# Performance work log

Measured on AMD Instinct MI355X. Metric: run time of the kernel, lower is better.

Reference implementation:

```python
import jax, jax.numpy as jnp
import numpy as np


def setup_inputs() -> dict:
    key = jax.random.key(0)
    k1, k2, k3 = jax.random.split(key, 3)
    N, F, C, E = 100000, 256, 64, 3200000
    x = jax.random.normal(k1, (N, F), dtype=jnp.float32)
    edge_index = jax.random.randint(k2, (2, E), 0, N, dtype=jnp.int64)
    W = jax.random.normal(k3, (F, C), dtype=jnp.float32) * (1.0 / np.sqrt(F))
    b = jnp.zeros((C,), dtype=jnp.float32)
    return {"x": x, "edge_index": edge_index, "W": W, "b": b}


def reference(x, edge_index, W, b):
    N = x.shape[0]
    # Linear transform first (GCNConv: x @ W)
    xw = x @ W  # [N, C]
    # gcn_norm: add self-loops with weight 1
    loops = jnp.arange(N, dtype=edge_index.dtype)
    src = jnp.concatenate([edge_index[0], loops])
    dst = jnp.concatenate([edge_index[1], loops])
    ones = jnp.ones(src.shape[0], dtype=xw.dtype)
    deg = jax.ops.segment_sum(ones, dst, num_segments=N)  # in-degree incl. self-loop
    deg_inv_sqrt = jnp.where(deg > 0, jax.lax.rsqrt(deg), 0.0)
    norm = deg_inv_sqrt[src] * deg_inv_sqrt[dst]  # [E+N]
    # Message: norm * x_j, then MEAN aggregation over destinations (aggr='mean')
    msg = xw[src] * norm[:, None]  # [E+N, C]
    agg = jax.ops.segment_sum(msg, dst, num_segments=N)  # [N, C]
    cnt = jnp.maximum(deg, 1.0)  # number of incoming messages per node
    out = agg / cnt[:, None] + b
    return jax.nn.log_softmax(out, axis=1)
```

## Files before the change

### kernel.cpp

```cpp
#include <hip/hip_runtime.h>


#define C_DIM 64
#define F_DIM 256
#define TILE 128
#define BIN_PT 16
#define BIN_TILE_E 4096
#define SORT_CAP 6144

typedef __attribute__((ext_vector_type(8))) short bf16x8;
typedef __attribute__((ext_vector_type(2))) short bf16x2;
typedef __attribute__((ext_vector_type(4))) float f32x4;

static __device__ __forceinline__ unsigned short f2bf(float f) {
    unsigned int u = __float_as_uint(f);
    unsigned int r = (u + 0x7FFFu + ((u >> 16) & 1u)) >> 16;
    return (unsigned short)r;
}
static __device__ __forceinline__ float u2lo(unsigned int u) {
    return __uint_as_float(u << 16);
}
static __device__ __forceinline__ float u2hi(unsigned int u) {
    return __uint_as_float(u & 0xFFFF0000u);
}

#if __has_builtin(__builtin_amdgcn_fdot2_f32_bf16)
static __device__ __forceinline__ void acc_pair(unsigned int u, float& lo, float& hi) {
    union { unsigned int ui; bf16x2 v; } p;
    p.ui = u;
    const bf16x2 SEL_LO = { (short)0x3F80, (short)0 };
    const bf16x2 SEL_HI = { (short)0, (short)0x3F80 };
    lo = __builtin_amdgcn_fdot2_f32_bf16(p.v, SEL_LO, lo, false);
    hi = __builtin_amdgcn_fdot2_f32_bf16(p.v, SEL_HI, hi, false);
}
#else
static __device__ __forceinline__ void acc_pair(unsigned int u, float& lo, float& hi) {
    lo += u2lo(u);
    hi += u2hi(u);
}
#endif


__global__ void k_zero1(int* __restrict__ a, int N) {
    int i = blockIdx.x * blockDim.x + threadIdx.x;
    if (i < N) a[i] = 0;
}

__global__ void k_zero2(int* __restrict__ a, int* __restrict__ b, int N) {
    int i = blockIdx.x * blockDim.x + threadIdx.x;
    if (i < N) { a[i] = 0; b[i] = 0; }
}

__global__ void k_count(const int* __restrict__ ei, int* __restrict__ degE, int E) {
    int stride = gridDim.x * blockDim.x;
    for (int e = blockIdx.x * blockDim.x + threadIdx.x; e < E; e += stride)
        atomicAdd(&degE[ei[E + e]], 1);
}

__global__ void k_dis2(const int* __restrict__ degE, float* __restrict__ dis, int N) {
    int i = blockIdx.x * blockDim.x + threadIdx.x;
    if (i < N) dis[i] = rsqrtf((float)(degE[i] + 1));
}


__global__ void k_prep(const float* __restrict__ W, unsigned short* __restrict__ Wt,
                       int* __restrict__ gcur, int K) {
    int i = blockIdx.x * blockDim.x + threadIdx.x;
    int c = i & 63, k = i >> 6;
    Wt[(size_t)c * F_DIM + k] = f2bf(W[(size_t)k * C_DIM + c]);
    if (i < K) gcur[i] = i * SORT_CAP;
}


__launch_bounds__(256)
__global__ void k_bin(const int* __restrict__ ei, int* __restrict__ gcur,
                      unsigned int* __restrict__ colb, int E, int K, int nTiles) {
    __shared__ int hcnt[1024];
    __shared__ int hoff[1024];
    __shared__ int gbase[1024];
    __shared__ int wps[4];
    __shared__ unsigned int stage[BIN_TILE_E];
    __shared__ unsigned short stage_bk[BIN_TILE_E];
    const int t = threadIdx.x;
    const int wv = t >> 6;
    const int ln = t & 63;

    for (int tile = blockIdx.x; tile < nTiles; tile += gridDim.x) {
        const int e0 = tile * BIN_TILE_E;
        const int nE = min(BIN_TILE_E, E - e0);
        hcnt[t] = 0; hcnt[t + 256] = 0; hcnt[t + 512] = 0; hcnt[t + 768] = 0;
        __syncthreads();

        unsigned int pk[BIN_PT];
        int bk[BIN_PT];
        int off[BIN_PT];
        #pragma unroll
        for (int j = 0; j < BIN_PT; ++j) {
            int e = e0 + j * 256 + t;
            if (e < E) {
                int s = ei[e];
                int d = ei[E + e];
                int k = d >> 7;
                bk[j]  = k;
                pk[j]  = ((unsigned)(d & 127) << 25) | (unsigned)s;
                off[j] = atomicAdd(&hcnt[k], 1);
            } else bk[j] = -1;
        }
        __syncthreads();

        int a0 = hcnt[t*4], a1 = hcnt[t*4+1], a2 = hcnt[t*4+2], a3 = hcnt[t*4+3];
        int s4 = a0 + a1 + a2 + a3;
        int incl = s4;
        #pragma unroll
        for (int o = 1; o < 64; o <<= 1) {
            int u = __shfl_up(incl, o, 64);
            if (ln >= o) incl += u;
        }
        if (ln == 63) wps[wv] = incl;
        __syncthreads();
        int wpre = 0;
        #pragma unroll
        for (int w = 0; w < 4; ++w)
            if (w < wv) wpre += wps[w];
        int eb = wpre + incl - s4;
        hoff[t*4+0] = eb;
        hoff[t*4+1] = eb + a0;
        hoff[t*4+2] = eb + a0 + a1;
        hoff[t*4+3] = eb + a0 + a1 + a2;
        __syncthreads();

        #pragma unroll
        for (int j = 0; j < BIN_PT; ++j)
            if (bk[j] >= 0) {
                int p = hoff[bk[j]] + off[j];
                stage[p] = pk[j];
                stage_bk[p] = (unsigned short)bk[j];
            }

        for (int kq = t; kq < K; kq += 256) {
            int c = hcnt[kq];
            gbase[kq] = (c > 0) ? atomicAdd(&gcur[kq], c) : 0;
        }
        __syncthreads();

        for (int i = t; i < nE; i += 256) {
            int bb = stage_bk[i];
            int idx = gbase[bb] + (i - hoff[bb]);
            if (idx < (bb + 1) * SORT_CAP)
                colb[idx] = stage[i];
        }
        __syncthreads();
    }
}


__launch_bounds__(256)
__global__ void k_sort(unsigned int* __restrict__ colb,
                       const int* __restrict__ gcur,
                       int* __restrict__ rowptr, int* __restrict__ rowcnt,
                       float* __restrict__ dis, int N, int K) {
    __shared__ unsigned int scache[SORT_CAP];
    __shared__ int ncnt[TILE];
    __shared__ int nscan[TILE];
    __shared__ int ncur[TILE];
    const int t = threadIdx.x;
    const int k = blockIdx.x;
    const int base = k * SORT_CAP;
    const int cnt  = min(gcur[k] - base, SORT_CAP);
    const int node0 = k << 7;

    if (t < TILE) ncnt[t] = 0;
    __syncthreads();
    for (int i = t; i < cnt; i += 256) {
        unsigned int pk = colb[base + i];
        scache[i] = pk;
        atomicAdd(&ncnt[pk >> 25], 1);
    }
    __syncthreads();

    if (t < TILE) nscan[t] = ncnt[t];
    __syncthreads();
    for (int o = 1; o < TILE; o <<= 1) {
        int v = 0;
        if (t < TILE && t >= o) v = nscan[t - o];
        __syncthreads();
        if (t < TILE) nscan[t] += v;
        __syncthreads();
    }
    if (t < TILE) {
        int ex = nscan[t] - ncnt[t];
        ncur[t] = ex;
        int node = node0 + t;
        if (node < N) {
            rowptr[node] = base + ex;
            rowcnt[node] = ncnt[t];
            dis[node] = rsqrtf((float)(ncnt[t] + 1));
        }
    }
    __syncthreads();

    for (int i = t; i < cnt; i += 256) {
        unsigned int pk = scache[i];
        int dl  = (int)(pk >> 25);
        int pos = atomicAdd(&ncur[dl], 1);
        colb[base + pos] = pk & 0x1FFFFFFu;
    }
}


__launch_bounds__(256)
__global__ void k_gemm_mfma(const float* __restrict__ x,
                            const unsigned short* __restrict__ Wt,
                            const float* __restrict__ dis,
                            unsigned short* __restrict__ yb, int N) {
    __shared__ float4 xs2[2][1024];
    const int t    = threadIdx.x;
    const int wv   = t >> 6;
    const int lane = t & 63;
    const int lr   = lane & 15;
    const int lq   = lane >> 4;
    const int row0 = blockIdx.x * 64;

    auto stage = [&](int buf, int kk) {
        #pragma unroll
        for (int j = 0; j < 4; ++j) {
            int base_idx = j * 256 + wv * 64;
            int idx = base_idx + lane;
            int r   = idx >> 4;
            int c4  = idx & 15;
            int sc4 = c4 ^ (r & 15);
            int gr  = row0 + r;
            if (gr >= N) gr = N - 1;
            const float* g = x + (size_t)gr * F_DIM + kk * 64 + sc4 * 4;
            float4* lbase = &xs2[buf][base_idx];
            __builtin_amdgcn_global_load_lds(
                (const __attribute__((address_space(1))) unsigned int*)g,
                (__attribute__((address_space(3))) unsigned int*)lbase,
                16, 0, 0);
        }
    };

    f32x4 acc[4] = {};

    stage(0, 0);
    __syncthreads();

    for (int kk = 0; kk < 4; ++kk) {
        if (kk < 3) stage((kk + 1) & 1, kk + 1);

        const float4* rowp = &xs2[kk & 1][(wv * 16 + lr) * 16];
        #pragma unroll
        for (int kc2 = 0; kc2 < 2; ++kc2) {
            int c4 = kc2 * 8 + lq * 2;
            float4 f0 = rowp[c4 ^ lr];
            float4 f1 = rowp[(c4 + 1) ^ lr];
            union { bf16x8 v; unsigned int u[4]; } a;
            a.u[0] = (unsigned)f2bf(f0.x) | ((unsigned)f2bf(f0.y) << 16);
            a.u[1] = (unsigned)f2bf(f0.z) | ((unsigned)f2bf(f0.w) << 16);
            a.u[2] = (unsigned)f2bf(f1.x) | ((unsigned)f2bf(f1.y) << 16);
            a.u[3] = (unsigned)f2bf(f1.z) | ((unsigned)f2bf(f1.w) << 16);
            const int kglob = kk * 64 + kc2 * 32 + lq * 8;
            #pragma unroll
            for (int cb = 0; cb < 4; ++cb) {
                bf16x8 bfr = *(const bf16x8*)(Wt + (size_t)(cb * 16 + lr) * F_DIM + kglob);
                acc[cb] = __builtin_amdgcn_mfma_f32_16x16x32_bf16(a.v, bfr, acc[cb], 0, 0, 0);
            }
        }
        __syncthreads();
    }

    const int rbase = row0 + wv * 16 + lq * 4;
    #pragma unroll
    for (int j = 0; j < 4; ++j) {
        int r = rbase + j;
        if (r < N) {
            float dd = dis[r];
            #pragma unroll
            for (int cb = 0; cb < 4; ++cb)
                yb[(size_t)r * C_DIM + cb * 16 + lr] = f2bf(acc[cb][j] * dd);
        }
    }
}


__launch_bounds__(256)
__global__ void k_agg(const int* __restrict__ rowptr, const int* __restrict__ rowcnt,
                      const int* __restrict__ col,
                      const uint4* __restrict__ yb8, const float* __restrict__ dis,
                      const float* __restrict__ b, float* __restrict__ out, int N) {
    const int lane = threadIdx.x & 63;
    const int g    = lane >> 3;
    const int cl   = lane & 7;
    int row = blockIdx.x * 4 + (threadIdx.x >> 6);
    if (row >= N) return;
    const int start = rowptr[row];
    const int cntE  = rowcnt[row];
    const int end   = start + cntE;

    float a0 = 0.f, a1 = 0.f, a2 = 0.f, a3 = 0.f;
    float a4 = 0.f, a5 = 0.f, a6 = 0.f, a7 = 0.f;
    if (g == 0) {
        uint4 u = yb8[(size_t)row * 8 + cl];
        a0 = u2lo(u.x); a1 = u2hi(u.x); a2 = u2lo(u.y); a3 = u2hi(u.y);
        a4 = u2lo(u.z); a5 = u2hi(u.z); a6 = u2lo(u.w); a7 = u2hi(u.w);
    }

    int i = start + g;
    for (; i + 24 < end; i += 32) {
        int s[4];
        #pragma unroll
        for (int j = 0; j < 4; ++j) s[j] = col[i + 8 * j];
        uint4 v[4];
        #pragma unroll
        for (int j = 0; j < 4; ++j) v[j] = yb8[(size_t)s[j] * 8 + cl];
        #pragma unroll
        for (int j = 0; j < 4; ++j) {
            acc_pair(v[j].x, a0, a1);
            acc_pair(v[j].y, a2, a3);
            acc_pair(v[j].z, a4, a5);
            acc_pair(v[j].w, a6, a7);
        }
    }
    for (; i + 8 < end; i += 16) {
        int s0 = col[i], s1 = col[i + 8];
        uint4 v0 = yb8[(size_t)s0 * 8 + cl];
        uint4 v1 = yb8[(size_t)s1 * 8 + cl];
        acc_pair(v0.x, a0, a1); acc_pair(v1.x, a0, a1);
        acc_pair(v0.y, a2, a3); acc_pair(v1.y, a2, a3);
        acc_pair(v0.z, a4, a5); acc_pair(v1.z, a4, a5);
        acc_pair(v0.w, a6, a7); acc_pair(v1.w, a6, a7);
    }
    for (; i < end; i += 8) {
        uint4 u = yb8[(size_t)col[i] * 8 + cl];
        acc_pair(u.x, a0, a1);
        acc_pair(u.y, a2, a3);
        acc_pair(u.z, a4, a5);
        acc_pair(u.w, a6, a7);
    }

    #pragma unroll
    for (int o = 8; o <= 32; o <<= 1) {
        a0 += __shfl_xor(a0, o, 64); a1 += __shfl_xor(a1, o, 64);
        a2 += __shfl_xor(a2, o, 64); a3 += __shfl_xor(a3, o, 64);
        a4 += __shfl_xor(a4, o, 64); a5 += __shfl_xor(a5, o, 64);
        a6 += __shfl_xor(a6, o, 64); a7 += __shfl_xor(a7, o, 64);
    }

    const float scale = dis[row] / (float)(cntE + 1);
    const float4 b0 = *(const float4*)&b[8 * cl];
    const float4 b1 = *(const float4*)&b[8 * cl + 4];
    float v0 = a0 * scale + b0.x;
    float v1 = a1 * scale + b0.y;
    float v2 = a2 * scale + b0.z;
    float v3 = a3 * scale + b0.w;
    float v4 = a4 * scale + b1.x;
    float v5 = a5 * scale + b1.y;
    float v6 = a6 * scale + b1.z;
    float v7 = a7 * scale + b1.w;

    float m = fmaxf(fmaxf(fmaxf(v0, v1), fmaxf(v2, v3)),
                    fmaxf(fmaxf(v4, v5), fmaxf(v6, v7)));
    #pragma unroll
    for (int o = 4; o >= 1; o >>= 1) m = fmaxf(m, __shfl_xor(m, o, 64));
    float ss = __expf(v0 - m) + __expf(v1 - m) + __expf(v2 - m) + __expf(v3 - m)
             + __expf(v4 - m) + __expf(v5 - m) + __expf(v6 - m) + __expf(v7 - m);
    #pragma unroll
    for (int o = 4; o >= 1; o >>= 1) ss += __shfl_xor(ss, o, 64);
    float lg = logf(ss);

    if (g == 0) {
        float* orow = out + (size_t)row * C_DIM + 8 * cl;
        *(float4*)(orow + 0) = make_float4(v0 - m - lg, v1 - m - lg, v2 - m - lg, v3 - m - lg);
        *(float4*)(orow + 4) = make_float4(v4 - m - lg, v5 - m - lg, v6 - m - lg, v7 - m - lg);
    }
}


__launch_bounds__(256, 4)
__global__ void k_gemmF(const float* __restrict__ x, const float* __restrict__ W,
                        const float* __restrict__ dis, float* __restrict__ y, int N) {
    __shared__ float xs[64 * 68];
    __shared__ float ws[64 * 64];
    const int t   = threadIdx.x;
    const int c16 = t & 15;
    const int rg  = t >> 4;
    const int row0 = blockIdx.x * 64;

    float acc[4][4] = {};

    for (int kk = 0; kk < F_DIM / 64; ++kk) {
        {
            int r  = t >> 2;
            int fq = (t & 3) * 16;
            int grow = row0 + r;
            float4 v0, v1, v2, v3;
            if (grow < N) {
                const float* src = x + (long long)grow * F_DIM + kk * 64 + fq;
                v0 = *(const float4*)(src + 0);
                v1 = *(const float4*)(src + 4);
                v2 = *(const float4*)(src + 8);
                v3 = *(const float4*)(src + 12);
            } else {
                v0 = v1 = v2 = v3 = make_float4(0.f, 0.f, 0.f, 0.f);
            }
            float4* dstp = (float4*)&xs[r * 68 + fq];
            dstp[0] = v0; dstp[1] = v1; dstp[2] = v2; dstp[3] = v3;
        }
        {
            int f  = t >> 2;
            int cq = (t & 3) * 16;
            const float* src = W + (long long)(kk * 64 + f) * C_DIM + cq;
            float4* dstp = (float4*)&ws[f * 64 + cq];
            dstp[0] = *(const float4*)(src + 0);
            dstp[1] = *(const float4*)(src + 4);
            dstp[2] = *(const float4*)(src + 8);
            dstp[3] = *(const float4*)(src + 12);
        }
        __syncthreads();

        const float4* xs4 = (const float4*)xs;
        const float4* ws4 = (const float4*)ws;
        #pragma unroll
        for (int f4 = 0; f4 < 16; ++f4) {
            float xr[4][4];
            #pragma unroll
            for (int k = 0; k < 4; ++k) {
                float4 v = xs4[(rg * 4 + k) * 17 + f4];
                xr[k][0] = v.x; xr[k][1] = v.y; xr[k][2] = v.z; xr[k][3] = v.w;
            }
            #pragma unroll
            for (int j = 0; j < 4; ++j) {
                float4 wv = ws4[(f4 * 4 + j) * 16 + c16];
                #pragma unroll
                for (int k = 0; k < 4; ++k) {
                    acc[k][0] += xr[k][j] * wv.x;
                    acc[k][1] += xr[k][j] * wv.y;
                    acc[k][2] += xr[k][j] * wv.z;
                    acc[k][3] += xr[k][j] * wv.w;
                }
            }
        }
        __syncthreads();
    }

    const int c = c16 * 4;
    #pragma unroll
    for (int k = 0; k < 4; ++k) {
        int row = row0 + rg * 4 + k;
        if (row < N) {
            float dd = dis[row];
            float4 v = make_float4(acc[k][0]*dd, acc[k][1]*dd, acc[k][2]*dd, acc[k][3]*dd);
            *(float4*)&y[(size_t)row * C_DIM + c] = v;
        }
    }
}

__global__ void k_scan_blk(const int* __restrict__ degE, int* __restrict__ excl,
                           int* __restrict__ bsum, int N) {
    __shared__ int sm[1024];
    const int tid = threadIdx.x;
    int i = blockIdx.x * 1024 + tid;
    int v = (i < N) ? degE[i] : 0;
    sm[tid] = v;
    __syncthreads();
    for (int off = 1; off < 1024; off <<= 1) {
        int t = (tid >= off) ? sm[tid - off] : 0;
        __syncthreads();
        sm[tid] += t;
        __syncthreads();
    }
    int incl = sm[tid];
    if (i < N) excl[i] = incl - v;
    if (tid == 1023) bsum[blockIdx.x] = incl;
}

__global__ void k_scan_top(int* __restrict__ bs, int nblk) {
    __shared__ int sm[128];
    const int tid = threadIdx.x;
    int v = (tid < nblk) ? bs[tid] : 0;
    sm[tid] = v;
    __syncthreads();
    for (int off = 1; off < 128; off <<= 1) {
        int t = (tid >= off) ? sm[tid - off] : 0;
        __syncthreads();
        sm[tid] += t;
        __syncthreads();
    }
    if (tid < nblk) bs[tid] = sm[tid] - v;
}

__global__ void k_scan_add(const int* __restrict__ excl, const int* __restrict__ bs,
                           int* __restrict__ rowptr, int N, int E) {
    int i = blockIdx.x * blockDim.x + threadIdx.x;
    if (i < N) rowptr[i] = excl[i] + bs[i >> 10];
    if (i == 0) rowptr[N] = E;
}

__global__ void k_scatter(const int* __restrict__ ei, const int* __restrict__ rowptr,
                          int* __restrict__ cnt, int* __restrict__ col, int E) {
    int stride = gridDim.x * blockDim.x;
    for (int e = blockIdx.x * blockDim.x + threadIdx.x; e < E; e += stride) {
        int s = ei[e];
        int d = ei[E + e];
        int p = atomicAdd(&cnt[d], 1);
        col[rowptr[d] + p] = s;
    }
}

__global__ void k_aggB(const int* __restrict__ rowptr, const int* __restrict__ col,
                       const float* __restrict__ y, const float* __restrict__ dis,
                       const float* __restrict__ b, float* __restrict__ out, int N) {
    const int lane = threadIdx.x & 63;
    int row = blockIdx.x * 4 + (threadIdx.x >> 6);
    if (row >= N) return;
    const int start = rowptr[row], end = rowptr[row + 1];
    float acc = y[(size_t)row * C_DIM + lane];
    for (int i = start; i < end; ++i) acc += y[(size_t)col[i] * C_DIM + lane];
    float val = acc * dis[row] / (float)(end - start + 1) + b[lane];
    float m = val;
    #pragma unroll
    for (int o = 32; o >= 1; o >>= 1) m = fmaxf(m, __shfl_xor(m, o, 64));
    float ex = expf(val - m);
    float ss = ex;
    #pragma unroll
    for (int o = 32; o >= 1; o >>= 1) ss += __shfl_xor(ss, o, 64);
    out[(size_t)row * C_DIM + lane] = val - m - logf(ss);
}

__global__ void k_selfloop2(const float* __restrict__ y, const float* __restrict__ dis,
                            float* __restrict__ agg, int NC) {
    int i = blockIdx.x * blockDim.x + threadIdx.x;
    if (i < NC) agg[i] = dis[i >> 6] * y[i];
}

__launch_bounds__(256)
__global__ void k_edge2(const int* __restrict__ ei, const float* __restrict__ y,
                        const float* __restrict__ dis, float* __restrict__ agg, int E) {
    const int lane = threadIdx.x & 63;
    int wid = (blockIdx.x * blockDim.x + threadIdx.x) >> 6;
    int nw  = (gridDim.x * blockDim.x) >> 6;
    for (int e = wid; e < E; e += nw) {
        int s = ei[e];
        int d = ei[E + e];
        atomicAdd(&agg[(size_t)d * C_DIM + lane], y[(size_t)s * C_DIM + lane] * dis[d]);
    }
}

__launch_bounds__(256)
__global__ void k_final2(float* __restrict__ agg, const int* __restrict__ degE,
                         const float* __restrict__ b, int N) {
    const int lane = threadIdx.x & 63;
    int row = blockIdx.x * 4 + (threadIdx.x >> 6);
    if (row >= N) return;
    float v = agg[(size_t)row * C_DIM + lane] / (float)(degE[row] + 1) + b[lane];
    float m = v;
    #pragma unroll
    for (int o = 32; o >= 1; o >>= 1) m = fmaxf(m, __shfl_xor(m, o, 64));
    float ex = expf(v - m);
    float ss = ex;
    #pragma unroll
    for (int o = 32; o >= 1; o >>= 1) ss += __shfl_xor(ss, o, 64);
    agg[(size_t)row * C_DIM + lane] = v - m - logf(ss);
}


extern "C" void kernel_launch(void* const* d_in, const int* in_sizes, int n_in,
                              void* d_out, int out_size, void* d_ws, size_t ws_size,
                              hipStream_t stream) {
    const float* x  = (const float*)d_in[0];
    const int*   ei = (const int*)d_in[1];
    const float* W  = (const float*)d_in[2];
    const float* b  = (const float*)d_in[3];

    const int C = in_sizes[3];
    const int F = in_sizes[2] / C;
    const int N = in_sizes[0] / F;
    const int E = in_sizes[1] / 2;

    float* out = (float*)d_out;
    char*  wsb = (char*)d_ws;

    const int K    = (N + TILE - 1) / TILE;
    const int nblk = (N + 1023) / 1024;

    size_t offA = 0;
    unsigned short* yb = (unsigned short*)(wsb + offA); offA += ((size_t)N * C * 2 + 15) & ~15ull;
    unsigned short* Wt = (unsigned short*)(wsb + offA); offA += ((size_t)F * C * 2 + 15) & ~15ull;
    float* disA   = (float*)(wsb + offA); offA += (size_t)N * 4;
    int*   rowptrA= (int*)(wsb + offA);   offA += (size_t)N * 4;
    int*   rowcntA= (int*)(wsb + offA);   offA += (size_t)N * 4;
    int*   gcur   = (int*)(wsb + offA);   offA += (size_t)K * 4;
    unsigned int* colb = (unsigned int*)(wsb + offA); offA += (size_t)K * SORT_CAP * 4;

    size_t offB = 0;
    float* yB     = (float*)(wsb + offB); offB += (size_t)N * C * 4;
    float* disB   = (float*)(wsb + offB); offB += (size_t)N * 4;
    int*   rowptrB= (int*)(wsb + offB);   offB += ((size_t)N + 1) * 4;
    int*   degE   = (int*)(wsb + offB);   offB += (size_t)N * 4;
    int*   cntB   = (int*)(wsb + offB);   offB += (size_t)N * 4;
    int*   excl   = (int*)(wsb + offB);   offB += (size_t)nblk * 1024 * 4;
    int*   bsum   = (int*)(wsb + offB);   offB += 128 * 4;
    int*   colB   = (int*)(wsb + offB);   offB += (size_t)E * 4;

    const bool okA = (offA <= ws_size) && (K <= 1024) && (N < (1 << 25)) &&
                     (C == 64) && (F == 256) &&
                     ((long long)E < (long long)K * SORT_CAP);
    const bool okB = (offB <= ws_size) && (nblk <= 128);

    const dim3 B256(256);
    const dim3 gN((N + 255) / 256);
    const int nTiles = (E + BIN_TILE_E - 1) / BIN_TILE_E;
    const int gemmBlocks = (N + 63) / 64;

    if (okA) {
        hipLaunchKernelGGL(k_prep,      dim3((F * C + 255) / 256), B256, 0, stream,
                           W, Wt, gcur, K);
        hipLaunchKernelGGL(k_bin,       dim3(nTiles), B256, 0, stream, ei, gcur, colb,
                           E, K, nTiles);
        hipLaunchKernelGGL(k_sort,      dim3(K), B256, 0, stream, colb, gcur,
                           rowptrA, rowcntA, disA, N, K);
        hipLaunchKernelGGL(k_gemm_mfma, dim3(gemmBlocks), B256, 0, stream, x, Wt, disA, yb, N);
        hipLaunchKernelGGL(k_agg,       dim3((N + 3) / 4), B256, 0, stream,
                           rowptrA, rowcntA, (const int*)colb,
                           (const uint4*)yb, disA, b, out, N);
    } else if (okB) {
        hipLaunchKernelGGL(k_zero2,    gN, B256, 0, stream, degE, cntB, N);
        hipLaunchKernelGGL(k_count,    dim3(2048), B256, 0, stream, ei, degE, E);
        hipLaunchKernelGGL(k_dis2,     gN, B256, 0, stream, degE, disB, N);
        hipLaunchKernelGGL(k_scan_blk, dim3(nblk), dim3(1024), 0, stream, degE, excl, bsum, N);
        hipLaunchKernelGGL(k_scan_top, dim3(1), dim3(128), 0, stream, bsum, nblk);
        hipLaunchKernelGGL(k_scan_add, gN, B256, 0, stream, excl, bsum, rowptrB, N, E);
        hipLaunchKernelGGL(k_gemmF,    dim3(gemmBlocks), B256, 0, stream, x, W, disB, yB, N);
        hipLaunchKernelGGL(k_scatter,  dim3(2048), B256, 0, stream, ei, rowptrB, cntB, colB, E);
        hipLaunchKernelGGL(k_aggB,     dim3((N + 3) / 4), B256, 0, stream,
                           rowptrB, colB, yB, disB, b, out, N);
    } else {
        hipLaunchKernelGGL(k_zero1,     gN, B256, 0, stream, degE, N);
        hipLaunchKernelGGL(k_count,     dim3(2048), B256, 0, stream, ei, degE, E);
        hipLaunchKernelGGL(k_dis2,      gN, B256, 0, stream, degE, disB, N);
        hipLaunchKernelGGL(k_gemmF,     dim3(gemmBlocks), B256, 0, stream, x, W, disB, yB, N);
        hipLaunchKernelGGL(k_selfloop2, dim3(((size_t)N * C + 255) / 256), B256, 0, stream,
                           yB, disB, out, N * C);
        hipLaunchKernelGGL(k_edge2,     dim3(4096), B256, 0, stream, ei, yB, disB, out, E);
        hipLaunchKernelGGL(k_final2,    dim3((N + 3) / 4), B256, 0, stream, out, degE, b, N);
    }
}
```

Before: 163.0 us.

## Merge edge binning and GEMM into one launch, apply degree scaling in sort

Edge binning and the x@W MFMA GEMM now run as disjoint block ranges of a single kernel, so the two independent stages can overlap on the GPU. The GEMM no longer waits for degree normalization. Instead, k_sort rescales the bf16 yb rows by dis after computing degrees. This adds an extra read-modify-write of yb (N×64 bf16) and a second bf16 rounding, in exchange for removing one launch and the serial dependency.

After: 160.0 us. About the same (-1.8%).

```diff
diff --git a/kernel.cpp b/kernel.cpp
--- a/kernel.cpp
+++ b/kernel.cpp
@@ -7,6 +7,7 @@
 #define BIN_PT 16
 #define BIN_TILE_E 4096
 #define SORT_CAP 6144
+#define SMEM_BYTES 36880
 
 typedef __attribute__((ext_vector_type(8))) short bf16x8;
 typedef __attribute__((ext_vector_type(2))) short bf16x2;
@@ -73,20 +74,26 @@
 
 
 __launch_bounds__(256)
-__global__ void k_bin(const int* __restrict__ ei, int* __restrict__ gcur,
-                      unsigned int* __restrict__ colb, int E, int K, int nTiles) {
-    __shared__ int hcnt[1024];
-    __shared__ int hoff[1024];
-    __shared__ int gbase[1024];
-    __shared__ int wps[4];
-    __shared__ unsigned int stage[BIN_TILE_E];
-    __shared__ unsigned short stage_bk[BIN_TILE_E];
+__global__ void k_bin_gemm(const int* __restrict__ ei, int* __restrict__ gcur,
+                           unsigned int* __restrict__ colb,
+                           const float* __restrict__ x,
+                           const unsigned short* __restrict__ Wt,
+                           unsigned short* __restrict__ yb,
+                           int E, int K, int nTiles, int N) {
+    __shared__ __align__(16) char smem[SMEM_BYTES];
     const int t = threadIdx.x;
-    const int wv = t >> 6;
-    const int ln = t & 63;
-
-    for (int tile = blockIdx.x; tile < nTiles; tile += gridDim.x) {
-        const int e0 = tile * BIN_TILE_E;
+
+    if (blockIdx.x < nTiles) {
+        int* hcnt  = (int*)smem;
+        int* hoff  = (int*)(smem + 4096);
+        int* gbase = (int*)(smem + 8192);
+        int* wps   = (int*)(smem + 12288);
+        unsigned int*  stage    = (unsigned int*)(smem + 12304);
+        unsigned short* stage_bk = (unsigned short*)(smem + 28688);
+        const int wv = t >> 6;
+        const int ln = t & 63;
+
+        const int e0 = blockIdx.x * BIN_TILE_E;
         const int nE = min(BIN_TILE_E, E - e0);
         hcnt[t] = 0; hcnt[t + 256] = 0; hcnt[t + 512] = 0; hcnt[t + 768] = 0;
         __syncthreads();
@@ -149,79 +156,17 @@
             if (idx < (bb + 1) * SORT_CAP)
                 colb[idx] = stage[i];
         }
-        __syncthreads();
-    }
-}
-
-
-__launch_bounds__(256)
-__global__ void k_sort(unsigned int* __restrict__ colb,
-                       const int* __restrict__ gcur,
-                       int* __restrict__ rowptr, int* __restrict__ rowcnt,
-                       float* __restrict__ dis, int N, int K) {
-    __shared__ unsigned int scache[SORT_CAP];
-    __shared__ int ncnt[TILE];
-    __shared__ int nscan[TILE];
-    __shared__ int ncur[TILE];
-    const int t = threadIdx.x;
-    const int k = blockIdx.x;
-    const int base = k * SORT_CAP;
-    const int cnt  = min(gcur[k] - base, SORT_CAP);
-    const int node0 = k << 7;
-
-    if (t < TILE) ncnt[t] = 0;
-    __syncthreads();
-    for (int i = t; i < cnt; i += 256) {
-        unsigned int pk = colb[base + i];
-        scache[i] = pk;
-        atomicAdd(&ncnt[pk >> 25], 1);
-    }
-    __syncthreads();
-
-    if (t < TILE) nscan[t] = ncnt[t];
-    __syncthreads();
-    for (int o = 1; o < TILE; o <<= 1) {
-        int v = 0;
-        if (t < TILE && t >= o) v = nscan[t - o];
-        __syncthreads();
-        if (t < TILE) nscan[t] += v;
-        __syncthreads();
-    }
-    if (t < TILE) {
-        int ex = nscan[t] - ncnt[t];
-        ncur[t] = ex;
-        int node = node0 + t;
-        if (node < N) {
-            rowptr[node] = base + ex;
-            rowcnt[node] = ncnt[t];
-            dis[node] = rsqrtf((float)(ncnt[t] + 1));
-        }
-    }
-    __syncthreads();
-
-    for (int i = t; i < cnt; i += 256) {
-        unsigned int pk = scache[i];
-        int dl  = (int)(pk >> 25);
-        int pos = atomicAdd(&ncur[dl], 1);
-        colb[base + pos] = pk & 0x1FFFFFFu;
-    }
-}
-
-
-__launch_bounds__(256)
-__global__ void k_gemm_mfma(const float* __restrict__ x,
-                            const unsigned short* __restrict__ Wt,
-                            const float* __restrict__ dis,
-                            unsigned short* __restrict__ yb, int N) {
-    __shared__ float4 xs2[2][1024];
-    const int t    = threadIdx.x;
+        return;
+    }
+
+    float4 (*xs2)[1024] = (float4 (*)[1024])smem;
     const int wv   = t >> 6;
     const int lane = t & 63;
     const int lr   = lane & 15;
     const int lq   = lane >> 4;
-    const int row0 = blockIdx.x * 64;
-
-    auto stage = [&](int buf, int kk) {
+    const int row0 = (blockIdx.x - nTiles) * 64;
+
+    auto stagefn = [&](int buf, int kk) {
         #pragma unroll
         for (int j = 0; j < 4; ++j) {
             int base_idx = j * 256 + wv * 64;
@@ -242,11 +187,11 @@
 
     f32x4 acc[4] = {};
 
-    stage(0, 0);
+    stagefn(0, 0);
     __syncthreads();
 
     for (int kk = 0; kk < 4; ++kk) {
-        if (kk < 3) stage((kk + 1) & 1, kk + 1);
+        if (kk < 3) stagefn((kk + 1) & 1, kk + 1);
 
         const float4* rowp = &xs2[kk & 1][(wv * 16 + lr) * 16];
         #pragma unroll
@@ -274,11 +219,80 @@
     for (int j = 0; j < 4; ++j) {
         int r = rbase + j;
         if (r < N) {
-            float dd = dis[r];
             #pragma unroll
             for (int cb = 0; cb < 4; ++cb)
-                yb[(size_t)r * C_DIM + cb * 16 + lr] = f2bf(acc[cb][j] * dd);
-        }
+                yb[(size_t)r * C_DIM + cb * 16 + lr] = f2bf(acc[cb][j]);
+        }
+    }
+}
+
+
+__launch_bounds__(256)
+__global__ void k_sort(unsigned int* __restrict__ colb,
+                       const int* __restrict__ gcur,
+                       int* __restrict__ rowptr, int* __restrict__ rowcnt,
+                       float* __restrict__ dis,
+                       unsigned int* __restrict__ yb2,
+                       int N, int K) {
+    __shared__ unsigned int scache[SORT_CAP];
+    __shared__ int ncnt[TILE];
+    __shared__ int nscan[TILE];
+    __shared__ int ncur[TILE];
+    __shared__ float sdis[TILE];
+    const int t = threadIdx.x;
+    const int k = blockIdx.x;
+    const int base = k * SORT_CAP;
+    const int cnt  = min(gcur[k] - base, SORT_CAP);
+    const int node0 = k << 7;
+
+    if (t < TILE) ncnt[t] = 0;
+    __syncthreads();
+    for (int i = t; i < cnt; i += 256) {
+        unsigned int pk = colb[base + i];
+        scache[i] = pk;
+        atomicAdd(&ncnt[pk >> 25], 1);
+    }
+    __syncthreads();
+
+    if (t < TILE) nscan[t] = ncnt[t];
+    __syncthreads();
+    for (int o = 1; o < TILE; o <<= 1) {
+        int v = 0;
+        if (t < TILE && t >= o) v = nscan[t - o];
+        __syncthreads();
+        if (t < TILE) nscan[t] += v;
+        __syncthreads();
+    }
+    if (t < TILE) {
+        int ex = nscan[t] - ncnt[t];
+        ncur[t] = ex;
+        int node = node0 + t;
+        if (node < N) {
+            rowptr[node] = base + ex;
+            rowcnt[node] = ncnt[t];
+            float d = rsqrtf((float)(ncnt[t] + 1));
+            dis[node] = d;
+            sdis[t] = d;
+        }
+    }
+    __syncthreads();
+
+    for (int i = t; i < cnt; i += 256) {
+        unsigned int pk = scache[i];
+        int dl  = (int)(pk >> 25);
+        int pos = atomicAdd(&ncur[dl], 1);
+        colb[base + pos] = pk & 0x1FFFFFFu;
+    }
+
+    const int nrows = min(TILE, N - node0);
+    unsigned int* yrow = yb2 + (size_t)node0 * 32;
+    for (int u = t; u < nrows * 32; u += 256) {
+        int r = u >> 5;
+        unsigned int v = yrow[u];
+        float d = sdis[r];
+        unsigned short lo = f2bf(u2lo(v) * d);
+        unsigned short hi = f2bf(u2hi(v) * d);
+        yrow[u] = ((unsigned int)hi << 16) | lo;
     }
 }
 
@@ -613,14 +627,13 @@
     const int gemmBlocks = (N + 63) / 64;
 
     if (okA) {
-        hipLaunchKernelGGL(k_prep,      dim3((F * C + 255) / 256), B256, 0, stream,
+        hipLaunchKernelGGL(k_prep,     dim3((F * C + 255) / 256), B256, 0, stream,
                            W, Wt, gcur, K);
-        hipLaunchKernelGGL(k_bin,       dim3(nTiles), B256, 0, stream, ei, gcur, colb,
-                           E, K, nTiles);
-        hipLaunchKernelGGL(k_sort,      dim3(K), B256, 0, stream, colb, gcur,
-                           rowptrA, rowcntA, disA, N, K);
-        hipLaunchKernelGGL(k_gemm_mfma, dim3(gemmBlocks), B256, 0, stream, x, Wt, disA, yb, N);
-        hipLaunchKernelGGL(k_agg,       dim3((N + 3) / 4), B256, 0, stream,
+        hipLaunchKernelGGL(k_bin_gemm, dim3(nTiles + gemmBlocks), B256, 0, stream,
+                           ei, gcur, colb, x, Wt, yb, E, K, nTiles, N);
+        hipLaunchKernelGGL(k_sort,     dim3(K), B256, 0, stream, colb, gcur,
+                           rowptrA, rowcntA, disA, (unsigned int*)yb, N, K);
+        hipLaunchKernelGGL(k_agg,      dim3((N + 3) / 4), B256, 0, stream,
                            rowptrA, rowcntA, (const int*)colb,
                            (const uint4*)yb, disA, b, out, N);
     } else if (okB) {
```
